# Kernel tuning notes

Hardware: AMD Instinct MI355X
Metric: run time of the kernel (lower is better)

## Reference

```python
import jax, jax.numpy as jnp
import numpy as np

N, E = 50000, 800000
IN_DIM, HID, OUT = 512, 128, 64
EPS = 0.3
N_LAYERS = 2


def setup_inputs() -> dict:
    key = jax.random.key(0)
    ks = jax.random.split(key, 10)
    src = jax.random.randint(ks[0], (E,), 0, N, dtype=jnp.int32)
    dst = jax.random.randint(ks[1], (E,), 0, N, dtype=jnp.int32)
    yes_no = jax.random.randint(ks[2], (E,), 0, 2, dtype=jnp.int32)
    # symmetric degree norm d = (deg+1)^-1/2 (self-loop-adjusted, as in DGL FAGCN)
    deg = jax.ops.segment_sum(jnp.ones((E,), jnp.float32), dst, num_segments=N)
    d = jax.lax.rsqrt(deg + 1.0)
    return {
        "h": jax.random.normal(ks[3], (N, IN_DIM), jnp.float32),
        "d": d,
        "t1_w": jax.random.normal(ks[4], (HID, IN_DIM), jnp.float32) * (1.414 / np.sqrt(IN_DIM)),
        "t1_b": jnp.zeros((HID,), jnp.float32),
        "gate_w": jax.random.normal(ks[5], (N_LAYERS, 2 * HID), jnp.float32) * (1.414 / np.sqrt(2 * HID)),
        "gate_b": jnp.zeros((N_LAYERS,), jnp.float32),
        "t2_w": jax.random.normal(ks[6], (OUT, HID), jnp.float32) * (1.414 / np.sqrt(HID)),
        "t2_b": jnp.zeros((OUT,), jnp.float32),
        "yes_weight": jnp.float32(1.5),
        "no_weight": jnp.float32(-0.5),
        "src": src,
        "dst": dst,
        "yes_no": yes_no,
    }


def reference(h, d, t1_w, t1_b, gate_w, gate_b, t2_w, t2_b, yes_weight, no_weight, src, dst, yes_no):
    n = h.shape[0]
    hdim = t1_w.shape[0]
    yn = yes_no.astype(h.dtype)
    # yes/no edge bias is layer-independent
    yn_term = jnp.tanh(yn * yes_weight + (1.0 - yn) * no_weight)  # [E]
    dd = d[dst] * d[src]  # [E]

    x = jax.nn.relu(h @ t1_w.T + t1_b)  # [N, H] (dropout is identity in eval)
    raw = x
    for i in range(gate_w.shape[0]):
        # gate(concat(h_dst, h_src)) == h@w_dst (gathered at dst) + h@w_src (gathered at src)
        gd = x @ gate_w[i, :hdim]   # [N]
        gs = x @ gate_w[i, hdim:]   # [N]
        g = jnp.tanh(gd[dst] + gs[src] + gate_b[i])  # [E]
        e = (g + yn_term) * 0.5 * dd                 # [E]
        msg = x[src] * e[:, None]                    # [E, H]
        z = jax.ops.segment_sum(msg, dst, num_segments=n)  # [N, H]
        x = EPS * raw + z
    logits = x @ t2_w.T + t2_b
    return jax.nn.log_softmax(logits, axis=1)
```

## Files before the change

### kernel.cpp

```cpp
#include <hip/hip_runtime.h>
#include <math.h>

#define N_NODES 50000
#define N_EDGES 800000
#define IN_DIM  512
#define HID     128
#define OUT_DIM 64
#define EPS     0.3f

#define LDS_ROW 516

typedef __attribute__((ext_vector_type(8))) short bf16x8;
typedef __attribute__((ext_vector_type(8))) __bf16 bf16v8;
typedef __attribute__((ext_vector_type(4))) float f32x4;

__device__ __forceinline__ float fast_tanh(float x) {
    return 1.0f - 2.0f / (__expf(2.0f * x) + 1.0f);
}

__device__ __forceinline__ unsigned short f2bfu(float f) {
    return __builtin_bit_cast(unsigned short, (__bf16)f);
}
__device__ __forceinline__ unsigned pk2(float lo, float hi) {
    return (unsigned)f2bfu(lo) | ((unsigned)f2bfu(hi) << 16);
}
__device__ __forceinline__ float bf_lo(unsigned u) { return __uint_as_float(u << 16); }
__device__ __forceinline__ float bf_hi(unsigned u) { return __uint_as_float(u & 0xffff0000u); }

__device__ __forceinline__ int deg_of(float dv) {
    return (int)(1.0f / (dv * dv) + 0.5f) - 1;
}


__global__ void prep_k(const float* __restrict__ d, int* __restrict__ rowptr,
                       int* __restrict__ cursor,
                       const float* __restrict__ w, unsigned short* __restrict__ wb) {
    int bid = blockIdx.x, tid = threadIdx.x;

    if (bid == 0) {
        int n0 = tid * 196;
        int cnt = (n0 + 196 <= N_NODES) ? 196 : (N_NODES - n0);
        int s = 0;
        for (int j = 0; j < cnt; j += 4) {
            float4 dv = *(const float4*)&d[n0 + j];
            s += deg_of(dv.x) + deg_of(dv.y) + deg_of(dv.z) + deg_of(dv.w);
        }
        int lane = tid & 63, wv = tid >> 6;
        int sc = s;
#pragma unroll
        for (int off = 1; off < 64; off <<= 1) {
            int t = __shfl_up(sc, off);
            if (lane >= off) sc += t;
        }
        __shared__ int wtot[4];
        if (lane == 63) wtot[wv] = sc;
        __syncthreads();
        int wof = 0;
        for (int w2 = 0; w2 < wv; w2++) wof += wtot[w2];
        int run = wof + (sc - s);
        for (int j = 0; j < cnt; j += 4) {
            float4 dv = *(const float4*)&d[n0 + j];
            int dg[4] = {deg_of(dv.x), deg_of(dv.y), deg_of(dv.z), deg_of(dv.w)};
#pragma unroll
            for (int q = 0; q < 4; q++) {
                rowptr[n0 + j + q] = run;
                cursor[n0 + j + q] = run;
                run += dg[q];
            }
        }
        if (tid == 0) rowptr[N_NODES] = wtot[0] + wtot[1] + wtot[2] + wtot[3];
        return;
    }

    int t = (bid - 1) * 256 + tid;
    int lane = t & 63;
    int ct   = (t >> 6) & 7;
    int ks   = t >> 9;
    int row  = ct * 16 + (lane & 15);
    int kb   = ks * 32 + (lane >> 4) * 8;
    const float* p = &w[(size_t)row * IN_DIM + kb];
    float4 v0 = *(const float4*)p, v1 = *(const float4*)(p + 4);
    uint4 pk;
    pk.x = pk2(v0.x, v0.y);
    pk.y = pk2(v0.z, v0.w);
    pk.z = pk2(v1.x, v1.y);
    pk.w = pk2(v1.z, v1.w);
    *(uint4*)&wb[(size_t)t * 8] = pk;
}


__launch_bounds__(256)
__global__ void t1fill_k(const float* __restrict__ h, const unsigned short* __restrict__ wb,
                         const float* __restrict__ bias, const float* __restrict__ gw0,
                         const float* __restrict__ d,
                         unsigned short* __restrict__ xb0, float4* __restrict__ gv0,
                         const int* __restrict__ src, const int* __restrict__ dst,
                         const int* __restrict__ yn, int* __restrict__ cursor,
                         int* __restrict__ csr) {
    __shared__ float At[16 * LDS_ROW];
    __shared__ float red[4][4][4][2];

    if (blockIdx.x & 1) {
        int e = (blockIdx.x >> 1) * 256 + threadIdx.x;
        int dv = dst[e];
        int pos = atomicAdd(&cursor[dv], 1);
        csr[pos] = src[e] | (yn[e] << 31);
        return;
    }

    int tid  = threadIdx.x;
    int lane = tid & 63;
    int wv   = tid >> 6;
    int l15  = lane & 15;
    int quad = lane >> 4;
    int rowb = (blockIdx.x >> 1) * 16;

#pragma unroll
    for (int i = 0; i < 8; ++i) {
        int c    = wv * 8 + i;
        int row  = c >> 1, half = c & 1;
        const float* gsrc = &h[(size_t)(rowb + row) * IN_DIM + half * 256 + lane * 4];
        float* ldst = &At[row * LDS_ROW + half * 256];
        __builtin_amdgcn_global_load_lds(
            (const __attribute__((address_space(1))) unsigned int*)gsrc,
            (__attribute__((address_space(3))) unsigned int*)ldst, 16, 0, 0);
    }
    __syncthreads();

    int ct0 = wv * 2;
    const unsigned short* bp = &wb[(size_t)lane * 8];
    const float* arp = &At[l15 * LDS_ROW + quad * 8];
    f32x4 acc[2];
    acc[0] = (f32x4){0.f, 0.f, 0.f, 0.f};
    acc[1] = (f32x4){0.f, 0.f, 0.f, 0.f};
#pragma unroll 4
    for (int ks = 0; ks < 16; ++ks) {
        float4 a0 = *(const float4*)(arp + ks * 32);
        float4 a1 = *(const float4*)(arp + ks * 32 + 4);
        bf16v8 av;
        av[0] = (__bf16)a0.x; av[1] = (__bf16)a0.y;
        av[2] = (__bf16)a0.z; av[3] = (__bf16)a0.w;
        av[4] = (__bf16)a1.x; av[5] = (__bf16)a1.y;
        av[6] = (__bf16)a1.z; av[7] = (__bf16)a1.w;
        bf16x8 af = __builtin_bit_cast(bf16x8, av);
        bf16x8 b0 = *(const bf16x8*)(bp + (size_t)(ks * 8 + ct0) * 512);
        bf16x8 b1 = *(const bf16x8*)(bp + (size_t)(ks * 8 + ct0 + 1) * 512);
        acc[0] = __builtin_amdgcn_mfma_f32_16x16x32_bf16(af, b0, acc[0], 0, 0, 0);
        acc[1] = __builtin_amdgcn_mfma_f32_16x16x32_bf16(af, b1, acc[1], 0, 0, 0);
    }

    float pd[4] = {0.f, 0.f, 0.f, 0.f}, ps[4] = {0.f, 0.f, 0.f, 0.f};
#pragma unroll
    for (int ct = 0; ct < 2; ++ct) {
        int o = (ct0 + ct) * 16 + l15;
        float b = bias[o];
        float wd = gw0[o], wsv = gw0[128 + o];
#pragma unroll
        for (int r = 0; r < 4; ++r) {
            float v = acc[ct][r] + b;
            v = v > 0.f ? v : 0.f;
            int node = rowb + quad * 4 + r;
            xb0[(size_t)node * HID + o] = f2bfu(v);
            pd[r] += v * wd; ps[r] += v * wsv;
        }
    }
#pragma unroll
    for (int m = 1; m < 16; m <<= 1) {
#pragma unroll
        for (int r = 0; r < 4; ++r) {
            pd[r] += __shfl_xor(pd[r], m);
            ps[r] += __shfl_xor(ps[r], m);
        }
    }
    if (l15 == 0) {
#pragma unroll
        for (int r = 0; r < 4; ++r) {
            red[wv][quad][r][0] = pd[r];
            red[wv][quad][r][1] = ps[r];
        }
    }
    __syncthreads();
    if (wv == 0 && lane < 16) {
        int q = lane >> 2, r = lane & 3;
        float sd = red[0][q][r][0] + red[1][q][r][0] + red[2][q][r][0] + red[3][q][r][0];
        float ss = red[0][q][r][1] + red[1][q][r][1] + red[2][q][r][1] + red[3][q][r][1];
        int n = rowb + lane;
        gv0[n] = make_float4(sd, ss, d[n], 0.f);
    }
}


__global__ void agg_k(const unsigned short* __restrict__ xb,
                      const unsigned short* __restrict__ rb,
                      const int* __restrict__ rowptr, const int* __restrict__ csr,
                      const float4* __restrict__ gv,
                      const float* __restrict__ gb, int layer,
                      const float* __restrict__ yw, const float* __restrict__ nw,
                      const float* __restrict__ gw_next,
                      float4* __restrict__ gv_out,
                      unsigned short* __restrict__ xb_out) {
    int t = blockIdx.x * blockDim.x + threadIdx.x;
    int nid = t >> 6, lane = t & 63;
    if (nid >= N_NODES) return;
    int l15 = lane & 15, eg = lane >> 4;
    float acc[8];
#pragma unroll
    for (int j = 0; j < 8; j++) acc[j] = 0.f;
    if (lane < 16) {
        uint4 rv = *(const uint4*)&rb[(size_t)nid * HID + l15 * 8];
        acc[0] = EPS * bf_lo(rv.x); acc[1] = EPS * bf_hi(rv.x);
        acc[2] = EPS * bf_lo(rv.y); acc[3] = EPS * bf_hi(rv.y);
        acc[4] = EPS * bf_lo(rv.z); acc[5] = EPS * bf_hi(rv.z);
        acc[6] = EPS * bf_lo(rv.w); acc[7] = EPS * bf_hi(rv.w);
    }
    float4 gn = gv[nid];
    float gdn = gn.x + gb[layer];
    float dn  = gn.z;
    float ty  = fast_tanh(yw[0]);
    float tno = fast_tanh(nw[0]);
    int e0 = rowptr[nid], e1 = rowptr[nid + 1];
    for (int b0 = e0; b0 < e1; b0 += 64) {
        int e = b0 + lane;
        float cf = 0.f; int sidx = 0;
        if (e < e1) {
            int p = csr[e];
            int s = p & 0x7fffffff;
            float4 g = gv[s];
            float ynt = (p < 0) ? ty : tno;
            cf = (fast_tanh(gdn + g.y) + ynt) * 0.5f * dn * g.z;
            sidx = s;
        }
        int trips = e1 - b0; if (trips > 64) trips = 64;
        float cfA = __shfl(cf, eg);
        int   sA  = __shfl(sidx, eg);
        uint4 vA  = *(const uint4*)&xb[(size_t)sA * HID + l15 * 8];
        for (int t4 = 0; t4 < trips; t4 += 4) {
            float cfB = 0.f; uint4 vB = make_uint4(0, 0, 0, 0);
            if (t4 + 4 < trips) {
                int nx = t4 + 4 + eg;
                cfB = __shfl(cf, nx);
                int sB = __shfl(sidx, nx);
                vB = *(const uint4*)&xb[(size_t)sB * HID + l15 * 8];
            }
            acc[0] += cfA * bf_lo(vA.x); acc[1] += cfA * bf_hi(vA.x);
            acc[2] += cfA * bf_lo(vA.y); acc[3] += cfA * bf_hi(vA.y);
            acc[4] += cfA * bf_lo(vA.z); acc[5] += cfA * bf_hi(vA.z);
            acc[6] += cfA * bf_lo(vA.w); acc[7] += cfA * bf_hi(vA.w);
            cfA = cfB; vA = vB;
        }
    }
#pragma unroll
    for (int j = 0; j < 8; j++) acc[j] += __shfl_xor(acc[j], 32);
#pragma unroll
    for (int j = 0; j < 8; j++) acc[j] += __shfl_xor(acc[j], 16);
    if (lane < 16) {
        uint4 pk;
        pk.x = pk2(acc[0], acc[1]);
        pk.y = pk2(acc[2], acc[3]);
        pk.z = pk2(acc[4], acc[5]);
        pk.w = pk2(acc[6], acc[7]);
        *(uint4*)&xb_out[(size_t)nid * HID + l15 * 8] = pk;
    }
    if (gw_next) {
        float pd = 0.f, psv = 0.f;
#pragma unroll
        for (int j = 0; j < 8; j++) {
            int o = l15 * 8 + j;
            pd  += acc[j] * gw_next[o];
            psv += acc[j] * gw_next[128 + o];
        }
#pragma unroll
        for (int m = 1; m < 16; m <<= 1) {
            pd  += __shfl_xor(pd, m);
            psv += __shfl_xor(psv, m);
        }
        if (lane == 0) gv_out[nid] = make_float4(pd, psv, dn, 0.f);
    }
}


__launch_bounds__(256)
__global__ void out_k(const unsigned short* __restrict__ xb, const float* __restrict__ w,
                      const float* __restrict__ bias, float* __restrict__ out) {
    __shared__ float As[64][132];
    __shared__ float Bs[64][132];
    int tid = threadIdx.x;
    int n0  = blockIdx.x * 64;
#pragma unroll
    for (int j = 0; j < 4; j++) {
        int c8 = tid + j * 256;
        int r = c8 >> 4, c = (c8 & 15) * 8;
        int gr = n0 + r;
        uint4 v = make_uint4(0, 0, 0, 0);
        if (gr < N_NODES) v = *(const uint4*)&xb[(size_t)gr * HID + c];
        *(float4*)&As[r][c]     = make_float4(bf_lo(v.x), bf_hi(v.x), bf_lo(v.y), bf_hi(v.y));
        *(float4*)&As[r][c + 4] = make_float4(bf_lo(v.z), bf_hi(v.z), bf_lo(v.w), bf_hi(v.w));
    }
#pragma unroll
    for (int j = 0; j < 8; j++) {
        int f4 = tid + j * 256;
        int r = f4 >> 5, c = (f4 & 31) * 4;
        *(float4*)&Bs[r][c] = *(const float4*)&w[r * HID + c];
    }
    __syncthreads();
    int tn = tid >> 4, to = tid & 15;
    float acc[4][4];
#pragma unroll
    for (int i = 0; i < 4; i++)
#pragma unroll
        for (int j = 0; j < 4; j++) acc[i][j] = 0.0f;
#pragma unroll 2
    for (int k = 0; k < HID; k += 4) {
        float4 av[4], bv[4];
#pragma unroll
        for (int i = 0; i < 4; i++) av[i] = *(const float4*)&As[tn + 16 * i][k];
#pragma unroll
        for (int j = 0; j < 4; j++) bv[j] = *(const float4*)&Bs[to + 16 * j][k];
#pragma unroll
        for (int i = 0; i < 4; i++)
#pragma unroll
            for (int j = 0; j < 4; j++) {
                acc[i][j] += av[i].x * bv[j].x;
                acc[i][j] += av[i].y * bv[j].y;
                acc[i][j] += av[i].z * bv[j].z;
                acc[i][j] += av[i].w * bv[j].w;
            }
    }
    float bj[4];
#pragma unroll
    for (int j = 0; j < 4; j++) bj[j] = bias[to + 16 * j];
#pragma unroll
    for (int i = 0; i < 4; i++) {
        float v[4];
        float m = -1e30f;
#pragma unroll
        for (int j = 0; j < 4; j++) { v[j] = acc[i][j] + bj[j]; m = fmaxf(m, v[j]); }
#pragma unroll
        for (int s = 1; s < 16; s <<= 1) m = fmaxf(m, __shfl_xor(m, s));
        float sum = 0.f;
#pragma unroll
        for (int j = 0; j < 4; j++) sum += __expf(v[j] - m);
#pragma unroll
        for (int s = 1; s < 16; s <<= 1) sum += __shfl_xor(sum, s);
        float lse = m + __logf(sum);
        int r = n0 + tn + 16 * i;
        if (r < N_NODES) {
#pragma unroll
            for (int j = 0; j < 4; j++) out[r * OUT_DIM + to + 16 * j] = v[j] - lse;
        }
    }
}


extern "C" void kernel_launch(void* const* d_in, const int* in_sizes, int n_in,
                              void* d_out, int out_size, void* d_ws, size_t ws_size,
                              hipStream_t stream) {
    const float* h    = (const float*)d_in[0];
    const float* d    = (const float*)d_in[1];
    const float* t1_w = (const float*)d_in[2];
    const float* t1_b = (const float*)d_in[3];
    const float* gw   = (const float*)d_in[4];
    const float* gb   = (const float*)d_in[5];
    const float* t2_w = (const float*)d_in[6];
    const float* t2_b = (const float*)d_in[7];
    const float* yw   = (const float*)d_in[8];
    const float* nw   = (const float*)d_in[9];
    const int* src    = (const int*)d_in[10];
    const int* dst    = (const int*)d_in[11];
    const int* yn     = (const int*)d_in[12];
    float* outp = (float*)d_out;

    char* ws = (char*)d_ws;
    size_t off = 0;
    auto alloc = [&](size_t bytes) {
        void* p = ws + off;
        off = (off + bytes + 255) & ~(size_t)255;
        return p;
    };
    unsigned short* xb0 = (unsigned short*)alloc((size_t)N_NODES * HID * 2);
    unsigned short* xb1 = (unsigned short*)alloc((size_t)N_NODES * HID * 2);
    unsigned short* xb2 = (unsigned short*)alloc((size_t)N_NODES * HID * 2);
    unsigned short* wb  = (unsigned short*)alloc((size_t)8192 * 8 * 2);
    float4* gv0   = (float4*)alloc((size_t)N_NODES * 16);
    float4* gv1   = (float4*)alloc((size_t)N_NODES * 16);
    int*   rowptr = (int*)alloc((size_t)(N_NODES + 1) * 4);
    int*   cursor = (int*)alloc((size_t)N_NODES * 4);
    int*   csr    = (int*)alloc((size_t)N_EDGES * 4);
    (void)ws_size; (void)n_in; (void)in_sizes; (void)out_size;

    prep_k<<<33, 256, 0, stream>>>(d, rowptr, cursor, t1_w, wb);

    t1fill_k<<<2 * (N_NODES / 16), 256, 0, stream>>>(h, wb, t1_b, gw, d, xb0, gv0,
                                                     src, dst, yn, cursor, csr);

    int wave_blocks = (N_NODES * 64 + 255) / 256;

    agg_k<<<wave_blocks, 256, 0, stream>>>(xb0, xb0, rowptr, csr, gv0, gb, 0,
                                           yw, nw, gw + 256, gv1, xb1);
    agg_k<<<wave_blocks, 256, 0, stream>>>(xb1, xb0, rowptr, csr, gv1, gb, 1,
                                           yw, nw, (const float*)nullptr,
                                           (float4*)nullptr, xb2);

    out_k<<<(N_NODES + 63) / 64, 256, 0, stream>>>(xb2, t2_w, t2_b, outp);
}
```

Measured before the change: 365.9 us.

## Fuse output projection and log-softmax into last aggregation; split gate vectors into SoA

The final linear layer and log-softmax now run inside the second aggregation kernel's epilogue, so the separate output kernel and the bf16 round trip of the final hidden state go away. The per-node float4 gate records are also split into separate gd/gs arrays, with d read directly. The edge gather now pulls two 4-byte values from separate arrays instead of one 16-byte record. The fused epilogue re-reads t2_w from global/L2 per wave and adds 16-way shuffle reductions for 16 outputs, which raises register pressure and ALU work in the agg kernel.

```diff
diff --git a/kernel.cpp b/kernel.cpp
--- a/kernel.cpp
+++ b/kernel.cpp
@@ -92,8 +92,8 @@
 __launch_bounds__(256)
 __global__ void t1fill_k(const float* __restrict__ h, const unsigned short* __restrict__ wb,
                          const float* __restrict__ bias, const float* __restrict__ gw0,
-                         const float* __restrict__ d,
-                         unsigned short* __restrict__ xb0, float4* __restrict__ gv0,
+                         unsigned short* __restrict__ xb0,
+                         float* __restrict__ gd0, float* __restrict__ gs0,
                          const int* __restrict__ src, const int* __restrict__ dst,
                          const int* __restrict__ yn, int* __restrict__ cursor,
                          int* __restrict__ csr) {
@@ -184,8 +184,8 @@
         int q = lane >> 2, r = lane & 3;
         float sd = red[0][q][r][0] + red[1][q][r][0] + red[2][q][r][0] + red[3][q][r][0];
         float ss = red[0][q][r][1] + red[1][q][r][1] + red[2][q][r][1] + red[3][q][r][1];
-        int n = rowb + lane;
-        gv0[n] = make_float4(sd, ss, d[n], 0.f);
+        gd0[rowb + lane] = sd;
+        gs0[rowb + lane] = ss;
     }
 }
 
@@ -193,12 +193,15 @@
 __global__ void agg_k(const unsigned short* __restrict__ xb,
                       const unsigned short* __restrict__ rb,
                       const int* __restrict__ rowptr, const int* __restrict__ csr,
-                      const float4* __restrict__ gv,
+                      const float* __restrict__ d,
+                      const float* __restrict__ gd, const float* __restrict__ gs,
                       const float* __restrict__ gb, int layer,
                       const float* __restrict__ yw, const float* __restrict__ nw,
                       const float* __restrict__ gw_next,
-                      float4* __restrict__ gv_out,
-                      unsigned short* __restrict__ xb_out) {
+                      float* __restrict__ gd_out, float* __restrict__ gs_out,
+                      unsigned short* __restrict__ xb_out,
+                      const float* __restrict__ t2w, const float* __restrict__ t2b,
+                      float* __restrict__ outp) {
     int t = blockIdx.x * blockDim.x + threadIdx.x;
     int nid = t >> 6, lane = t & 63;
     if (nid >= N_NODES) return;
@@ -213,9 +216,8 @@
         acc[4] = EPS * bf_lo(rv.z); acc[5] = EPS * bf_hi(rv.z);
         acc[6] = EPS * bf_lo(rv.w); acc[7] = EPS * bf_hi(rv.w);
     }
-    float4 gn = gv[nid];
-    float gdn = gn.x + gb[layer];
-    float dn  = gn.z;
+    float gdn = gd[nid] + gb[layer];
+    float dn  = d[nid];
     float ty  = fast_tanh(yw[0]);
     float tno = fast_tanh(nw[0]);
     int e0 = rowptr[nid], e1 = rowptr[nid + 1];
@@ -225,9 +227,8 @@
         if (e < e1) {
             int p = csr[e];
             int s = p & 0x7fffffff;
-            float4 g = gv[s];
             float ynt = (p < 0) ? ty : tno;
-            cf = (fast_tanh(gdn + g.y) + ynt) * 0.5f * dn * g.z;
+            cf = (fast_tanh(gdn + gs[s]) + ynt) * 0.5f * dn * d[s];
             sidx = s;
         }
         int trips = e1 - b0; if (trips > 64) trips = 64;
@@ -253,15 +254,16 @@
     for (int j = 0; j < 8; j++) acc[j] += __shfl_xor(acc[j], 32);
 #pragma unroll
     for (int j = 0; j < 8; j++) acc[j] += __shfl_xor(acc[j], 16);
-    if (lane < 16) {
-        uint4 pk;
-        pk.x = pk2(acc[0], acc[1]);
-        pk.y = pk2(acc[2], acc[3]);
-        pk.z = pk2(acc[4], acc[5]);
-        pk.w = pk2(acc[6], acc[7]);
-        *(uint4*)&xb_out[(size_t)nid * HID + l15 * 8] = pk;
-    }
-    if (gw_next) {
+
+    if (!t2w) {
+        if (lane < 16) {
+            uint4 pk;
+            pk.x = pk2(acc[0], acc[1]);
+            pk.y = pk2(acc[2], acc[3]);
+            pk.z = pk2(acc[4], acc[5]);
+            pk.w = pk2(acc[6], acc[7]);
+            *(uint4*)&xb_out[(size_t)nid * HID + l15 * 8] = pk;
+        }
         float pd = 0.f, psv = 0.f;
 #pragma unroll
         for (int j = 0; j < 8; j++) {
@@ -274,80 +276,48 @@
             pd  += __shfl_xor(pd, m);
             psv += __shfl_xor(psv, m);
         }
-        if (lane == 0) gv_out[nid] = make_float4(pd, psv, dn, 0.f);
-    }
-}
-
-
-__launch_bounds__(256)
-__global__ void out_k(const unsigned short* __restrict__ xb, const float* __restrict__ w,
-                      const float* __restrict__ bias, float* __restrict__ out) {
-    __shared__ float As[64][132];
-    __shared__ float Bs[64][132];
-    int tid = threadIdx.x;
-    int n0  = blockIdx.x * 64;
-#pragma unroll
-    for (int j = 0; j < 4; j++) {
-        int c8 = tid + j * 256;
-        int r = c8 >> 4, c = (c8 & 15) * 8;
-        int gr = n0 + r;
-        uint4 v = make_uint4(0, 0, 0, 0);
-        if (gr < N_NODES) v = *(const uint4*)&xb[(size_t)gr * HID + c];
-        *(float4*)&As[r][c]     = make_float4(bf_lo(v.x), bf_hi(v.x), bf_lo(v.y), bf_hi(v.y));
-        *(float4*)&As[r][c + 4] = make_float4(bf_lo(v.z), bf_hi(v.z), bf_lo(v.w), bf_hi(v.w));
-    }
-#pragma unroll
-    for (int j = 0; j < 8; j++) {
-        int f4 = tid + j * 256;
-        int r = f4 >> 5, c = (f4 & 31) * 4;
-        *(float4*)&Bs[r][c] = *(const float4*)&w[r * HID + c];
-    }
-    __syncthreads();
-    int tn = tid >> 4, to = tid & 15;
-    float acc[4][4];
-#pragma unroll
-    for (int i = 0; i < 4; i++)
-#pragma unroll
-        for (int j = 0; j < 4; j++) acc[i][j] = 0.0f;
-#pragma unroll 2
-    for (int k = 0; k < HID; k += 4) {
-        float4 av[4], bv[4];
-#pragma unroll
-        for (int i = 0; i < 4; i++) av[i] = *(const float4*)&As[tn + 16 * i][k];
-#pragma unroll
-        for (int j = 0; j < 4; j++) bv[j] = *(const float4*)&Bs[to + 16 * j][k];
-#pragma unroll
-        for (int i = 0; i < 4; i++)
-#pragma unroll
-            for (int j = 0; j < 4; j++) {
-                acc[i][j] += av[i].x * bv[j].x;
-                acc[i][j] += av[i].y * bv[j].y;
-                acc[i][j] += av[i].z * bv[j].z;
-                acc[i][j] += av[i].w * bv[j].w;
-            }
-    }
-    float bj[4];
-#pragma unroll
-    for (int j = 0; j < 4; j++) bj[j] = bias[to + 16 * j];
-#pragma unroll
-    for (int i = 0; i < 4; i++) {
-        float v[4];
-        float m = -1e30f;
-#pragma unroll
-        for (int j = 0; j < 4; j++) { v[j] = acc[i][j] + bj[j]; m = fmaxf(m, v[j]); }
-#pragma unroll
-        for (int s = 1; s < 16; s <<= 1) m = fmaxf(m, __shfl_xor(m, s));
-        float sum = 0.f;
-#pragma unroll
-        for (int j = 0; j < 4; j++) sum += __expf(v[j] - m);
-#pragma unroll
-        for (int s = 1; s < 16; s <<= 1) sum += __shfl_xor(sum, s);
-        float lse = m + __logf(sum);
-        int r = n0 + tn + 16 * i;
-        if (r < N_NODES) {
-#pragma unroll
-            for (int j = 0; j < 4; j++) out[r * OUT_DIM + to + 16 * j] = v[j] - lse;
-        }
+        if (lane == 0) { gd_out[nid] = pd; gs_out[nid] = psv; }
+        return;
+    }
+
+    float p[16];
+    const float* wrow = t2w + (size_t)(eg * 16) * HID + l15 * 8;
+#pragma unroll
+    for (int oi = 0; oi < 16; oi++) {
+        float4 w0 = *(const float4*)(wrow + oi * HID);
+        float4 w1 = *(const float4*)(wrow + oi * HID + 4);
+        p[oi] = acc[0] * w0.x + acc[1] * w0.y + acc[2] * w0.z + acc[3] * w0.w
+              + acc[4] * w1.x + acc[5] * w1.y + acc[6] * w1.z + acc[7] * w1.w;
+    }
+#pragma unroll
+    for (int m = 1; m < 16; m <<= 1)
+#pragma unroll
+        for (int oi = 0; oi < 16; oi++) p[oi] += __shfl_xor(p[oi], m);
+    float4 bq0 = *(const float4*)&t2b[eg * 16];
+    float4 bq1 = *(const float4*)&t2b[eg * 16 + 4];
+    float4 bq2 = *(const float4*)&t2b[eg * 16 + 8];
+    float4 bq3 = *(const float4*)&t2b[eg * 16 + 12];
+    p[0] += bq0.x; p[1] += bq0.y; p[2]  += bq0.z; p[3]  += bq0.w;
+    p[4] += bq1.x; p[5] += bq1.y; p[6]  += bq1.z; p[7]  += bq1.w;
+    p[8] += bq2.x; p[9] += bq2.y; p[10] += bq2.z; p[11] += bq2.w;
+    p[12] += bq3.x; p[13] += bq3.y; p[14] += bq3.z; p[15] += bq3.w;
+    float mx = p[0];
+#pragma unroll
+    for (int oi = 1; oi < 16; oi++) mx = fmaxf(mx, p[oi]);
+    mx = fmaxf(mx, __shfl_xor(mx, 16));
+    mx = fmaxf(mx, __shfl_xor(mx, 32));
+    float ssum = 0.f;
+#pragma unroll
+    for (int oi = 0; oi < 16; oi++) ssum += __expf(p[oi] - mx);
+    ssum += __shfl_xor(ssum, 16);
+    ssum += __shfl_xor(ssum, 32);
+    float lse = mx + __logf(ssum);
+    if (l15 == 0) {
+        float* op = &outp[(size_t)nid * OUT_DIM + eg * 16];
+        *(float4*)(op)      = make_float4(p[0] - lse,  p[1] - lse,  p[2] - lse,  p[3] - lse);
+        *(float4*)(op + 4)  = make_float4(p[4] - lse,  p[5] - lse,  p[6] - lse,  p[7] - lse);
+        *(float4*)(op + 8)  = make_float4(p[8] - lse,  p[9] - lse,  p[10] - lse, p[11] - lse);
+        *(float4*)(op + 12) = make_float4(p[12] - lse, p[13] - lse, p[14] - lse, p[15] - lse);
     }
 }
 
@@ -379,10 +349,11 @@
     };
     unsigned short* xb0 = (unsigned short*)alloc((size_t)N_NODES * HID * 2);
     unsigned short* xb1 = (unsigned short*)alloc((size_t)N_NODES * HID * 2);
-    unsigned short* xb2 = (unsigned short*)alloc((size_t)N_NODES * HID * 2);
     unsigned short* wb  = (unsigned short*)alloc((size_t)8192 * 8 * 2);
-    float4* gv0   = (float4*)alloc((size_t)N_NODES * 16);
-    float4* gv1   = (float4*)alloc((size_t)N_NODES * 16);
+    float* gd0    = (float*)alloc((size_t)N_NODES * 4);
+    float* gs0    = (float*)alloc((size_t)N_NODES * 4);
+    float* gd1    = (float*)alloc((size_t)N_NODES * 4);
+    float* gs1    = (float*)alloc((size_t)N_NODES * 4);
     int*   rowptr = (int*)alloc((size_t)(N_NODES + 1) * 4);
     int*   cursor = (int*)alloc((size_t)N_NODES * 4);
     int*   csr    = (int*)alloc((size_t)N_EDGES * 4);
@@ -390,16 +361,18 @@
 
     prep_k<<<33, 256, 0, stream>>>(d, rowptr, cursor, t1_w, wb);
 
-    t1fill_k<<<2 * (N_NODES / 16), 256, 0, stream>>>(h, wb, t1_b, gw, d, xb0, gv0,
+    t1fill_k<<<2 * (N_NODES / 16), 256, 0, stream>>>(h, wb, t1_b, gw, xb0, gd0, gs0,
                                                      src, dst, yn, cursor, csr);
 
     int wave_blocks = (N_NODES * 64 + 255) / 256;
 
-    agg_k<<<wave_blocks, 256, 0, stream>>>(xb0, xb0, rowptr, csr, gv0, gb, 0,
-                                           yw, nw, gw + 256, gv1, xb1);
-    agg_k<<<wave_blocks, 256, 0, stream>>>(xb1, xb0, rowptr, csr, gv1, gb, 1,
+    agg_k<<<wave_blocks, 256, 0, stream>>>(xb0, xb0, rowptr, csr, d, gd0, gs0, gb, 0,
+                                           yw, nw, gw + 256, gd1, gs1, xb1,
+                                           (const float*)nullptr, (const float*)nullptr,
+                                           (float*)nullptr);
+    agg_k<<<wave_blocks, 256, 0, stream>>>(xb1, xb0, rowptr, csr, d, gd1, gs1, gb, 1,
                                            yw, nw, (const float*)nullptr,
-                                           (float4*)nullptr, xb2);
-
-    out_k<<<(N_NODES + 63) / 64, 256, 0, stream>>>(xb2, t2_w, t2_b, outp);
-}
+                                           (float*)nullptr, (float*)nullptr,
+                                           (unsigned short*)nullptr,
+                                           t2_w, t2_b, outp);
+}
```

New measurement: 461.7 us. +26.2%, slower.
